# Kernel optimization log

Hardware: AMD Instinct MI355X
Metric: run time of the kernel (lower is better)

## Reference

```python
import jax, jax.numpy as jnp
import numpy as np

B, T, D, R = 8, 4096, 768, 16
DB = D // 3  # bucket size (d_img = d_sym = 256, d_rf = D - 2*DB = 256)


def setup_inputs() -> dict:
    key = jax.random.key(0)
    ks = jax.random.split(key, 10)
    s = 0.05
    x = jax.random.normal(ks[0], (B, T, D), dtype=jnp.float32)
    # torch nn.Linear stores weight as (out, in); y = x @ W.T + b
    V_w = jax.random.normal(ks[1], (R, D), dtype=jnp.float32) * s
    U_w = jax.random.normal(ks[2], (D, R), dtype=jnp.float32) * s
    E1_w = jax.random.normal(ks[3], (DB, D), dtype=jnp.float32) * s
    E1_b = jnp.zeros((DB,), dtype=jnp.float32)
    E2_w = jax.random.normal(ks[4], (3, DB), dtype=jnp.float32) * s
    E2_b = jnp.zeros((3,), dtype=jnp.float32)
    # a_base init per bucket: img=-0.6, sym=-1.0, rf=-1.6; a_delta init 0 (perturbed so tanh path is exercised)
    a_base = jnp.concatenate([
        jnp.full((DB,), -0.6, dtype=jnp.float32),
        jnp.full((DB,), -1.0, dtype=jnp.float32),
        jnp.full((D - 2 * DB,), -1.6, dtype=jnp.float32),
    ])
    a_delta = jax.random.normal(ks[5], (D,), dtype=jnp.float32) * 0.1
    C_w = jax.random.normal(ks[6], (D, D), dtype=jnp.float32) * s
    G_w = jax.random.normal(ks[7], (D, D), dtype=jnp.float32) * s
    G_b = jnp.zeros((D,), dtype=jnp.float32)
    return {"x": x, "V_w": V_w, "U_w": U_w, "E1_w": E1_w, "E1_b": E1_b,
            "E2_w": E2_w, "E2_b": E2_b, "a_base": a_base, "a_delta": a_delta,
            "C_w": C_w, "G_w": G_w, "G_b": G_b}


def reference(x, V_w, U_w, E1_w, E1_b, E2_w, E2_b, a_base, a_delta, C_w, G_w, G_b):
    d = x.shape[-1]
    db = d // 3
    # Low-rank input projection: Bu = U(V(x))
    Z = jnp.einsum('btd,rd->btr', x, V_w)            # (B,T,R)
    Bu = jnp.einsum('btr,dr->btd', Z, U_w)           # (B,T,D)
    # Evidence scores per timestep (3 clinical buckets)
    h = jax.nn.gelu(jnp.einsum('btd,ed->bte', x, E1_w) + E1_b, approximate=False)
    alpha = jax.nn.sigmoid(jnp.einsum('bte,ce->btc', h, E2_w) + E2_b)  # (B,T,3)
    # Broadcast each bucket's evidence score over its channels
    alpha_rep = jnp.concatenate([
        jnp.broadcast_to(alpha[..., 0:1], alpha.shape[:-1] + (db,)),
        jnp.broadcast_to(alpha[..., 1:2], alpha.shape[:-1] + (db,)),
        jnp.broadcast_to(alpha[..., 2:3], alpha.shape[:-1] + (d - 2 * db,)),
    ], axis=-1)                                       # (B,T,D)
    a_eff = a_base + alpha_rep * jnp.tanh(a_delta)    # (B,T,D)
    lam = jnp.exp(-jax.nn.softplus(-a_eff))           # (B,T,D), in (0,1)
    # Diagonal linear recurrence s_t = lam_t * s_{t-1} + Bu_t  (scan over time)
    def step(s, inp):
        l_t, bu_t = inp
        s = l_t * s + bu_t
        return s, s
    s0 = jnp.zeros(x.shape[:1] + x.shape[2:], dtype=x.dtype)  # (B,D)
    _, S = jax.lax.scan(step, s0, (jnp.swapaxes(lam, 0, 1), jnp.swapaxes(Bu, 0, 1)))
    S = jnp.swapaxes(S, 0, 1)                         # (B,T,D)
    y = jnp.einsum('btd,od->bto', S, C_w)
    gate = jax.nn.sigmoid(jnp.einsum('btd,od->bto', x, G_w) + G_b)
    y = jax.nn.gelu(y, approximate=False) * gate
    return x + y  # dropout is identity in eval mode
```

## Files before the change

kernel.cpp:

```cpp
#include <hip/hip_runtime.h>
#include <hip/hip_bf16.h>
#include <math.h>

#define B_   8
#define T_   4096
#define D_   768
#define R_   16
#define DB_  256
#define N_   (B_ * T_)
#define NC_  64
#define L_   (T_ / NC_)
#define NKS_ (D_ / 32)
#define BUF_  12288
#define BUFE_ 8192

typedef __attribute__((ext_vector_type(8))) short bf16x8;
typedef __attribute__((ext_vector_type(4))) float f32x4;

__device__ __forceinline__ float gelu_exact(float x) {
    return 0.5f * x * (1.0f + erff(x * 0.70710678118654752f));
}
__device__ __forceinline__ float sigmoidf_(float x) {
    return 1.0f / (1.0f + expf(-x));
}
__device__ __forceinline__ float bf2f(unsigned short u) {
    return __uint_as_float(((unsigned)u) << 16);
}
__device__ __forceinline__ unsigned short f2bf(float f) {
    __hip_bfloat16 h = __float2bfloat16(f);
    return *(unsigned short*)&h;
}
__device__ __forceinline__ bf16x8 pack8(float4 a, float4 b) {
    bf16x8 r;
    r[0] = (short)f2bf(a.x); r[1] = (short)f2bf(a.y);
    r[2] = (short)f2bf(a.z); r[3] = (short)f2bf(a.w);
    r[4] = (short)f2bf(b.x); r[5] = (short)f2bf(b.y);
    r[6] = (short)f2bf(b.z); r[7] = (short)f2bf(b.w);
    return r;
}

__device__ __forceinline__ void gload16(const unsigned short* g, unsigned short* l) {
    __builtin_amdgcn_global_load_lds(
        (const __attribute__((address_space(1))) unsigned int*)(const void*)g,
        (__attribute__((address_space(3))) unsigned int*)(void*)l,
        16, 0, 0);
}

__device__ __forceinline__ bf16x8 frag_read(const unsigned short* lds, int row, int lq) {
    int q = lq ^ ((row >> 1) & 3);
    return *(const bf16x8*)(lds + row * 32 + q * 8);
}

__device__ __forceinline__ void tile_decode(int nwg, int ncol, int& rowt, int& colt) {
    int bid = blockIdx.x;
    int cpx = nwg >> 3;
    int swz = (bid & 7) * cpx + (bid >> 3);
    colt = swz % ncol;
    rowt = swz / ncol;
}

__device__ __forceinline__ void stage_a(const unsigned short* src, int row0, int k0,
                                        unsigned short* lds, int w, int l) {
#pragma unroll
    for (int j = 0; j < 2; ++j) {
        int i = ((w * 2 + j) << 6) + l;
        int row = i >> 2, q = i & 3;
        int qs = q ^ ((row >> 1) & 3);
        gload16(src + (size_t)(row0 + row) * D_ + k0 + qs * 8, lds + ((w * 2 + j) << 9));
    }
}
__device__ __forceinline__ void stage_b(const unsigned short* src, int col0, int k0,
                                        unsigned short* lds, int w, int l) {
    int i = (w << 6) + l;
    int row = i >> 2, q = i & 3;
    int qs = q ^ ((row >> 1) & 3);
    gload16(src + (size_t)(col0 + row) * D_ + k0 + qs * 8, lds + (w << 9));
}

__device__ __forceinline__ void tile_mfma44(const unsigned short* la, const unsigned short* lb,
                                            int wrow, int wcol, int lr, int lq,
                                            f32x4 acc[4][4]) {
    bf16x8 a[4], b[4];
#pragma unroll
    for (int m = 0; m < 4; m++) a[m] = frag_read(la, wrow + m * 16 + lr, lq);
#pragma unroll
    for (int n = 0; n < 4; n++) b[n] = frag_read(lb, wcol + n * 16 + lr, lq);
    __builtin_amdgcn_s_setprio(1);
#pragma unroll
    for (int m = 0; m < 4; m++)
#pragma unroll
        for (int n = 0; n < 4; n++)
            acc[m][n] = __builtin_amdgcn_mfma_f32_16x16x32_bf16(a[m], b[n], acc[m][n], 0, 0, 0);
    __builtin_amdgcn_s_setprio(0);
}

__device__ __forceinline__ void prologueF(const unsigned short* __restrict__ A,
                                          const unsigned short* __restrict__ Bm,
                                          int row0, int col0,
                                          unsigned short* lds, int w, int l) {
    stage_a(A,  row0, 0,  lds,                w, l);
    stage_b(Bm, col0, 0,  lds + 8192,         w, l);
    stage_a(A,  row0, 32, lds + BUF_,         w, l);
    stage_b(Bm, col0, 32, lds + BUF_ + 8192,  w, l);
}

template <bool DO_PROLOGUE>
__device__ __forceinline__ void kloopF(const unsigned short* __restrict__ A,
                                       const unsigned short* __restrict__ Bm,
                                       int row0, int col0,
                                       unsigned short* lds,
                                       int w, int l, f32x4 acc[4][4]) {
    const int lr = l & 15, lq = l >> 4;
    const int wrow = (w >> 1) * 64, wcol = (w & 1) * 64;

    if (DO_PROLOGUE) prologueF(A, Bm, row0, col0, lds, w, l);

#pragma unroll 3
    for (int t = 0; t < NKS_ - 2; ++t) {
        asm volatile("s_waitcnt vmcnt(3)" ::: "memory");
        __builtin_amdgcn_s_barrier();
        __builtin_amdgcn_sched_barrier(0);
        unsigned short* bn = lds + ((t + 2) % 3) * BUF_;
        stage_a(A,  row0, (t + 2) * 32, bn,        w, l);
        stage_b(Bm, col0, (t + 2) * 32, bn + 8192, w, l);
        unsigned short* bc = lds + (t % 3) * BUF_;
        tile_mfma44(bc, bc + 8192, wrow, wcol, lr, lq, acc);
    }
    asm volatile("s_waitcnt vmcnt(3)" ::: "memory");
    __builtin_amdgcn_s_barrier();
    __builtin_amdgcn_sched_barrier(0);
    {
        unsigned short* bc = lds + ((NKS_ - 2) % 3) * BUF_;
        tile_mfma44(bc, bc + 8192, wrow, wcol, lr, lq, acc);
    }
    asm volatile("s_waitcnt vmcnt(0)" ::: "memory");
    __builtin_amdgcn_s_barrier();
    __builtin_amdgcn_sched_barrier(0);
    {
        unsigned short* bc = lds + ((NKS_ - 1) % 3) * BUF_;
        tile_mfma44(bc, bc + 8192, wrow, wcol, lr, lq, acc);
    }
}

__global__ __launch_bounds__(512, 2)
void gemm_fused_out(const unsigned short* __restrict__ Xb,
                    const unsigned short* __restrict__ Gwb,
                    const unsigned short* __restrict__ Sb,
                    const unsigned short* __restrict__ Cwb,
                    const float* __restrict__ Gbias,
                    float* __restrict__ out) {
    __shared__ unsigned short lds[3 * BUF_];
    const int t = threadIdx.x, l = t & 63, w = t >> 6;
    int rowt, colt;
    tile_decode(768, 6, rowt, colt);
    const int row0 = rowt * 256, col0 = colt * 128;
    const int lr = l & 15, lq = l >> 4;
    const int wrow = (w >> 1) * 64, wcol = (w & 1) * 64;

    float gb[4];
#pragma unroll
    for (int n = 0; n < 4; n++) gb[n] = Gbias[col0 + wcol + n * 16 + lr];

    f32x4 acc[4][4] = {};
    kloopF<true>(Xb, Gwb, row0, col0, lds, w, l, acc);

    prologueF(Sb, Cwb, row0, col0, lds, w, l);

    unsigned int gp[4][4][2];
#pragma unroll
    for (int m = 0; m < 4; m++)
#pragma unroll
        for (int n = 0; n < 4; n++) {
            gp[m][n][0] = (unsigned)f2bf(sigmoidf_(acc[m][n][0] + gb[n]))
                        | ((unsigned)f2bf(sigmoidf_(acc[m][n][1] + gb[n])) << 16);
            gp[m][n][1] = (unsigned)f2bf(sigmoidf_(acc[m][n][2] + gb[n]))
                        | ((unsigned)f2bf(sigmoidf_(acc[m][n][3] + gb[n])) << 16);
            acc[m][n] = (f32x4){0.f, 0.f, 0.f, 0.f};
        }

    kloopF<false>(Sb, Cwb, row0, col0, lds, w, l, acc);

#pragma unroll
    for (int m = 0; m < 4; m++)
#pragma unroll
        for (int n = 0; n < 4; n++) {
            int col = col0 + wcol + n * 16 + lr;
#pragma unroll
            for (int r = 0; r < 4; r++) {
                int row = row0 + wrow + m * 16 + lq * 4 + r;
                size_t o = (size_t)row * D_ + col;
                float g = bf2f((unsigned short)(gp[m][n][r >> 1] >> ((r & 1) * 16)));
                out[o] = bf2f(Xb[o]) + gelu_exact(acc[m][n][r]) * g;
            }
        }
}

__device__ __forceinline__ void stage_e(const unsigned short* __restrict__ A,
                                        const unsigned short* __restrict__ Bm,
                                        int row0, int col0, int k0,
                                        unsigned short* buf, int w, int l) {
    int i = (w << 6) + l;
    int row = i >> 2, q = i & 3;
    int qs = q ^ ((row >> 1) & 3);
    gload16(A  + (size_t)(row0 + row) * D_ + k0 + qs * 8, buf + (w << 9));
    gload16(Bm + (size_t)(col0 + row) * D_ + k0 + qs * 8, buf + 4096 + (w << 9));
}

__device__ __forceinline__ void tile_mfma24(const unsigned short* buf,
                                            int wrow, int wcol, int lr, int lq,
                                            f32x4 acc[2][4]) {
    const unsigned short* la = buf;
    const unsigned short* lb = buf + 4096;
    bf16x8 a[2], b[4];
#pragma unroll
    for (int m = 0; m < 2; m++) a[m] = frag_read(la, wrow + m * 16 + lr, lq);
#pragma unroll
    for (int n = 0; n < 4; n++) b[n] = frag_read(lb, wcol + n * 16 + lr, lq);
    __builtin_amdgcn_s_setprio(1);
#pragma unroll
    for (int m = 0; m < 2; m++)
#pragma unroll
        for (int n = 0; n < 4; n++)
            acc[m][n] = __builtin_amdgcn_mfma_f32_16x16x32_bf16(a[m], b[n], acc[m][n], 0, 0, 0);
    __builtin_amdgcn_s_setprio(0);
}

__device__ __forceinline__ void kloopE(const unsigned short* __restrict__ A,
                                       const unsigned short* __restrict__ Bm,
                                       int row0, int col0,
                                       unsigned short* lds,
                                       int w, int l, f32x4 acc[2][4]) {
    const int lr = l & 15, lq = l >> 4;
    const int wrow = (w >> 1) * 32, wcol = (w & 1) * 64;

    stage_e(A, Bm, row0, col0, 0,  lds,             w, l);
    stage_e(A, Bm, row0, col0, 32, lds + BUFE_,     w, l);
    stage_e(A, Bm, row0, col0, 64, lds + 2 * BUFE_, w, l);

#pragma unroll 4
    for (int t = 0; t < NKS_ - 3; ++t) {
        asm volatile("s_waitcnt vmcnt(4)" ::: "memory");
        __builtin_amdgcn_s_barrier();
        __builtin_amdgcn_sched_barrier(0);
        stage_e(A, Bm, row0, col0, (t + 3) * 32, lds + ((t + 3) & 3) * BUFE_, w, l);
        tile_mfma24(lds + (t & 3) * BUFE_, wrow, wcol, lr, lq, acc);
    }
    asm volatile("s_waitcnt vmcnt(4)" ::: "memory");
    __builtin_amdgcn_s_barrier();
    __builtin_amdgcn_sched_barrier(0);
    tile_mfma24(lds + ((NKS_ - 3) & 3) * BUFE_, wrow, wcol, lr, lq, acc);
    asm volatile("s_waitcnt vmcnt(2)" ::: "memory");
    __builtin_amdgcn_s_barrier();
    __builtin_amdgcn_sched_barrier(0);
    tile_mfma24(lds + ((NKS_ - 2) & 3) * BUFE_, wrow, wcol, lr, lq, acc);
    asm volatile("s_waitcnt vmcnt(0)" ::: "memory");
    __builtin_amdgcn_s_barrier();
    __builtin_amdgcn_sched_barrier(0);
    tile_mfma24(lds + ((NKS_ - 1) & 3) * BUFE_, wrow, wcol, lr, lq, acc);
}

__global__ __launch_bounds__(512, 2)
void gemm_e1_alpha(const unsigned short* __restrict__ Xb,
                   const unsigned short* __restrict__ Wb,
                   const float* __restrict__ bias,
                   const float* __restrict__ E2w,
                   float* __restrict__ alpha_acc) {
    __shared__ unsigned short lds[4 * BUFE_];
    const int t = threadIdx.x, l = t & 63, w = t >> 6;
    int rowt, colt;
    tile_decode(512, 2, rowt, colt);
    const int row0 = rowt * 128, col0 = colt * 128;
    const int lr = l & 15, lq = l >> 4;
    const int wrow = (w >> 1) * 32, wcol = (w & 1) * 64;
    f32x4 acc[2][4] = {};
    kloopE(Xb, Wb, row0, col0, lds, w, l, acc);

    float bia[4], e2v[3][4];
#pragma unroll
    for (int n = 0; n < 4; n++) {
        int col = col0 + wcol + n * 16 + lr;
        bia[n] = bias[col];
#pragma unroll
        for (int c = 0; c < 3; c++) e2v[c][n] = E2w[c * DB_ + col];
    }
#pragma unroll
    for (int m = 0; m < 2; m++)
#pragma unroll
        for (int r = 0; r < 4; r++) {
            float p0 = 0.f, p1 = 0.f, p2 = 0.f;
#pragma unroll
            for (int n = 0; n < 4; n++) {
                float h = gelu_exact(acc[m][n][r] + bia[n]);
                p0 = fmaf(h, e2v[0][n], p0);
                p1 = fmaf(h, e2v[1][n], p1);
                p2 = fmaf(h, e2v[2][n], p2);
            }
#pragma unroll
            for (int s = 1; s < 16; s <<= 1) {
                p0 += __shfl_xor(p0, s);
                p1 += __shfl_xor(p1, s);
                p2 += __shfl_xor(p2, s);
            }
            if (lr == 0) {
                int row = row0 + wrow + m * 16 + lq * 4 + r;
                atomicAdd(&alpha_acc[(size_t)row * 3 + 0], p0);
                atomicAdd(&alpha_acc[(size_t)row * 3 + 1], p1);
                atomicAdd(&alpha_acc[(size_t)row * 3 + 2], p2);
            }
        }
}

#define SEG_E1  (DB_ * D_ / 4)
#define SEG_W   (D_ * D_ / 4)
#define SEG_Z   (N_ * 3 / 4)
#define SEG_TOT (SEG_E1 + 2 * SEG_W + SEG_Z + 192)

__global__ __launch_bounds__(256)
void cvtz_kernel(const float* __restrict__ X, const float* __restrict__ Vw,
                 unsigned short* __restrict__ Xb, float* __restrict__ Z,
                 const float* __restrict__ E1_w, const float* __restrict__ C_w,
                 const float* __restrict__ G_w, const float* __restrict__ a_delta,
                 unsigned short* __restrict__ E1b, unsigned short* __restrict__ Cwb,
                 unsigned short* __restrict__ Gwb, float* __restrict__ al_acc,
                 float* __restrict__ tanhd) {
    const int t = threadIdx.x, l = t & 63, w = t >> 6;
    const int lr = l & 15, lq = l >> 4;
    const int tok0 = (blockIdx.x * 4 + w) * 16;
    const float* xrow = X  + (size_t)(tok0 + lr) * D_;
    const float* vrow = Vw + (size_t)lr * D_;
    f32x4 acc = {};
#pragma unroll 4
    for (int k0 = 0; k0 < D_; k0 += 32) {
        int k = k0 + lq * 8;
        float4 xa = *(const float4*)&xrow[k];
        float4 xb = *(const float4*)&xrow[k + 4];
        float4 va = *(const float4*)&vrow[k];
        float4 vb = *(const float4*)&vrow[k + 4];
        bf16x8 xf = pack8(xa, xb);
        bf16x8 vf = pack8(va, vb);
        *(bf16x8*)&Xb[(size_t)(tok0 + lr) * D_ + k] = xf;
        acc = __builtin_amdgcn_mfma_f32_16x16x32_bf16(xf, vf, acc, 0, 0, 0);
    }
#pragma unroll
    for (int rr = 0; rr < 4; rr++)
        Z[(size_t)(tok0 + lq * 4 + rr) * R_ + lr] = acc[rr];

    for (int i = blockIdx.x * 256 + t; i < SEG_TOT; i += 512 * 256) {
        if (i < SEG_E1) {
            float4 v = ((const float4*)E1_w)[i];
            ((ushort4*)E1b)[i] = make_ushort4(f2bf(v.x), f2bf(v.y), f2bf(v.z), f2bf(v.w));
        } else if (i < SEG_E1 + SEG_W) {
            int j = i - SEG_E1;
            float4 v = ((const float4*)C_w)[j];
            ((ushort4*)Cwb)[j] = make_ushort4(f2bf(v.x), f2bf(v.y), f2bf(v.z), f2bf(v.w));
        } else if (i < SEG_E1 + 2 * SEG_W) {
            int j = i - SEG_E1 - SEG_W;
            float4 v = ((const float4*)G_w)[j];
            ((ushort4*)Gwb)[j] = make_ushort4(f2bf(v.x), f2bf(v.y), f2bf(v.z), f2bf(v.w));
        } else if (i < SEG_E1 + 2 * SEG_W + SEG_Z) {
            int j = i - SEG_E1 - 2 * SEG_W;
            ((float4*)al_acc)[j] = make_float4(0.f, 0.f, 0.f, 0.f);
        } else {
            int j = (i - SEG_E1 - 2 * SEG_W - SEG_Z) * 4;
            tanhd[j + 0] = tanhf(a_delta[j + 0]);
            tanhd[j + 1] = tanhf(a_delta[j + 1]);
            tanhd[j + 2] = tanhf(a_delta[j + 2]);
            tanhd[j + 3] = tanhf(a_delta[j + 3]);
        }
    }
}

__device__ __forceinline__ void load_chunk_lds768(const float* __restrict__ Z,
                                                  const float* __restrict__ al_acc,
                                                  const float* __restrict__ E2b,
                                                  int tok0, int t,
                                                  float* Zs, float* als) {
    if (t < L_ * R_ / 4)
        ((float4*)Zs)[t] = ((const float4*)&Z[(size_t)tok0 * R_])[t];
    if (t < L_ * 3)
        als[t] = sigmoidf_(al_acc[(size_t)tok0 * 3 + t] + E2b[t % 3]);
}

__device__ __forceinline__ float dot16(const float* zrow, const float4* u) {
    float4 z0 = *(const float4*)&zrow[0],  z1 = *(const float4*)&zrow[4];
    float4 z2 = *(const float4*)&zrow[8],  z3 = *(const float4*)&zrow[12];
    return z0.x*u[0].x + z0.y*u[0].y + z0.z*u[0].z + z0.w*u[0].w
         + z1.x*u[1].x + z1.y*u[1].y + z1.z*u[1].z + z1.w*u[1].w
         + z2.x*u[2].x + z2.y*u[2].y + z2.z*u[2].z + z2.w*u[2].w
         + z3.x*u[3].x + z3.y*u[3].y + z3.z*u[3].z + z3.w*u[3].w;
}

__global__ __launch_bounds__(768, 2)
void scan_pass1(const float* __restrict__ Z, const float* __restrict__ al_acc,
                const float* __restrict__ E2b,
                const float* __restrict__ Uw, const float* __restrict__ a_base,
                const float* __restrict__ tanhd,
                float* __restrict__ Aagg, float* __restrict__ Send) {
    __shared__ float Zs[L_ * R_];
    __shared__ float als[L_ * 3];
    const int t = threadIdx.x;
    const int c = blockIdx.x & (NC_ - 1);
    const int b = blockIdx.x >> 6;
    const int tok0 = b * T_ + c * L_;
    const int buck = t >> 8;
    load_chunk_lds768(Z, al_acc, E2b, tok0, t, Zs, als);

    float4 u[4];
#pragma unroll
    for (int q = 0; q < 4; q++)
        u[q] = *(const float4*)&Uw[(size_t)t * R_ + q * 4];
    float ab = a_base[t];
    float td = tanhd[t];
    __syncthreads();

    float a = 1.f, s = 0.f;
    for (int i = 0; i < L_; i++) {
        float av  = als[i * 3 + buck];
        float lam = sigmoidf_(fmaf(av, td, ab));
        float bu  = dot16(&Zs[i * R_], u);
        a *= lam;
        s = fmaf(lam, s, bu);
    }
    size_t o = ((size_t)(b * NC_ + c)) * D_ + t;
    Aagg[o] = a;
    Send[o] = s;
}

__global__ __launch_bounds__(768, 2)
void scan_pass3(const float* __restrict__ Z, const float* __restrict__ al_acc,
                const float* __restrict__ E2b,
                const float* __restrict__ Uw, const float* __restrict__ a_base,
                const float* __restrict__ tanhd,
                const float* __restrict__ Aagg, const float* __restrict__ Send,
                unsigned short* __restrict__ Sout) {
    __shared__ float Zs[L_ * R_];
    __shared__ float als[L_ * 3];
    const int t = threadIdx.x;
    const int c = blockIdx.x & (NC_ - 1);
    const int b = blockIdx.x >> 6;
    const int tok0 = b * T_ + c * L_;
    const int buck = t >> 8;
    load_chunk_lds768(Z, al_acc, E2b, tok0, t, Zs, als);

    float4 u[4];
#pragma unroll
    for (int q = 0; q < 4; q++)
        u[q] = *(const float4*)&Uw[(size_t)t * R_ + q * 4];
    float ab = a_base[t];
    float td = tanhd[t];

    float s = 0.f;
#pragma unroll 4
    for (int cc = 0; cc < c; ++cc) {
        size_t o = ((size_t)(b * NC_ + cc)) * D_ + t;
        s = fmaf(Aagg[o], s, Send[o]);
    }
    __syncthreads();

    for (int i = 0; i < L_; i++) {
        float av  = als[i * 3 + buck];
        float lam = sigmoidf_(fmaf(av, td, ab));
        float bu  = dot16(&Zs[i * R_], u);
        s = fmaf(lam, s, bu);
        Sout[(size_t)(tok0 + i) * D_ + t] = f2bf(s);
    }
}

extern "C" void kernel_launch(void* const* d_in, const int* in_sizes, int n_in,
                              void* d_out, int out_size, void* d_ws, size_t ws_size,
                              hipStream_t stream) {
    const float* x       = (const float*)d_in[0];
    const float* V_w     = (const float*)d_in[1];
    const float* U_w     = (const float*)d_in[2];
    const float* E1_w    = (const float*)d_in[3];
    const float* E1_b    = (const float*)d_in[4];
    const float* E2_w    = (const float*)d_in[5];
    const float* E2_b    = (const float*)d_in[6];
    const float* a_base  = (const float*)d_in[7];
    const float* a_delta = (const float*)d_in[8];
    const float* C_w     = (const float*)d_in[9];
    const float* G_w     = (const float*)d_in[10];
    const float* G_b     = (const float*)d_in[11];
    float* out = (float*)d_out;

    char* p = (char*)d_ws;
    float* Aagg   = (float*)p;          p += (size_t)B_ * NC_ * D_ * 4;
    float* Send   = (float*)p;          p += (size_t)B_ * NC_ * D_ * 4;
    float* tanhd  = (float*)p;          p += (size_t)D_ * 4;
    float* Z      = (float*)p;          p += (size_t)N_ * R_ * 4;
    float* al_acc = (float*)p;          p += (size_t)N_ * 3 * 4;
    unsigned short* x_bf  = (unsigned short*)p; p += (size_t)N_ * D_ * 2;
    unsigned short* S_bf  = (unsigned short*)p; p += (size_t)N_ * D_ * 2;
    unsigned short* E1_bf = (unsigned short*)p; p += (size_t)DB_ * D_ * 2;
    unsigned short* Cw_bf = (unsigned short*)p; p += (size_t)D_ * D_ * 2;
    unsigned short* Gw_bf = (unsigned short*)p; p += (size_t)D_ * D_ * 2;

    cvtz_kernel<<<N_ / 64, 256, 0, stream>>>(x, V_w, x_bf, Z,
                                             E1_w, C_w, G_w, a_delta,
                                             E1_bf, Cw_bf, Gw_bf, al_acc, tanhd);

    gemm_e1_alpha<<<512, 512, 0, stream>>>(x_bf, E1_bf, E1_b, E2_w, al_acc);

    scan_pass1<<<B_ * NC_, 768, 0, stream>>>(Z, al_acc, E2_b, U_w, a_base, tanhd, Aagg, Send);
    scan_pass3<<<B_ * NC_, 768, 0, stream>>>(Z, al_acc, E2_b, U_w, a_base, tanhd, Aagg, Send, S_bf);

    gemm_fused_out<<<768, 512, 0, stream>>>(x_bf, Gw_bf, S_bf, Cw_bf, G_b, out);
}
```

Baseline: 276.6 us.

## Fuse two-pass chunked scan into one kernel with inter-block flag synchronization

Merges the chunk-aggregate pass and the carry-propagate pass of the time scan into a single kernel. Each block publishes its chunk aggregate, sets a flag, then spins until all earlier chunks of the same batch are flagged before computing its carry and writing the outputs. Flags are zeroed in the conversion kernel. This removes one kernel launch and the re-load of Z/alpha into LDS, but it relies on all 512 blocks being co-resident (768 threads, 2 per CU) to avoid deadlock, and it adds spin-wait latency.

```diff
diff --git a/kernel.cpp b/kernel.cpp
--- a/kernel.cpp
+++ b/kernel.cpp
@@ -313,7 +313,8 @@
 #define SEG_E1  (DB_ * D_ / 4)
 #define SEG_W   (D_ * D_ / 4)
 #define SEG_Z   (N_ * 3 / 4)
-#define SEG_TOT (SEG_E1 + 2 * SEG_W + SEG_Z + 192)
+#define SEG_F   (B_ * NC_ / 4)
+#define SEG_TOT (SEG_E1 + 2 * SEG_W + SEG_Z + SEG_F + 192)
 
 __global__ __launch_bounds__(256)
 void cvtz_kernel(const float* __restrict__ X, const float* __restrict__ Vw,
@@ -322,7 +323,7 @@
                  const float* __restrict__ G_w, const float* __restrict__ a_delta,
                  unsigned short* __restrict__ E1b, unsigned short* __restrict__ Cwb,
                  unsigned short* __restrict__ Gwb, float* __restrict__ al_acc,
-                 float* __restrict__ tanhd) {
+                 int* __restrict__ flags, float* __restrict__ tanhd) {
     const int t = threadIdx.x, l = t & 63, w = t >> 6;
     const int lr = l & 15, lq = l >> 4;
     const int tok0 = (blockIdx.x * 4 + w) * 16;
@@ -360,8 +361,11 @@
         } else if (i < SEG_E1 + 2 * SEG_W + SEG_Z) {
             int j = i - SEG_E1 - 2 * SEG_W;
             ((float4*)al_acc)[j] = make_float4(0.f, 0.f, 0.f, 0.f);
+        } else if (i < SEG_E1 + 2 * SEG_W + SEG_Z + SEG_F) {
+            int j = i - SEG_E1 - 2 * SEG_W - SEG_Z;
+            ((int4*)flags)[j] = make_int4(0, 0, 0, 0);
         } else {
-            int j = (i - SEG_E1 - 2 * SEG_W - SEG_Z) * 4;
+            int j = (i - SEG_E1 - 2 * SEG_W - SEG_Z - SEG_F) * 4;
             tanhd[j + 0] = tanhf(a_delta[j + 0]);
             tanhd[j + 1] = tanhf(a_delta[j + 1]);
             tanhd[j + 2] = tanhf(a_delta[j + 2]);
@@ -391,47 +395,12 @@
 }
 
 __global__ __launch_bounds__(768, 2)
-void scan_pass1(const float* __restrict__ Z, const float* __restrict__ al_acc,
+void scan_fused(const float* __restrict__ Z, const float* __restrict__ al_acc,
                 const float* __restrict__ E2b,
                 const float* __restrict__ Uw, const float* __restrict__ a_base,
                 const float* __restrict__ tanhd,
-                float* __restrict__ Aagg, float* __restrict__ Send) {
-    __shared__ float Zs[L_ * R_];
-    __shared__ float als[L_ * 3];
-    const int t = threadIdx.x;
-    const int c = blockIdx.x & (NC_ - 1);
-    const int b = blockIdx.x >> 6;
-    const int tok0 = b * T_ + c * L_;
-    const int buck = t >> 8;
-    load_chunk_lds768(Z, al_acc, E2b, tok0, t, Zs, als);
-
-    float4 u[4];
-#pragma unroll
-    for (int q = 0; q < 4; q++)
-        u[q] = *(const float4*)&Uw[(size_t)t * R_ + q * 4];
-    float ab = a_base[t];
-    float td = tanhd[t];
-    __syncthreads();
-
-    float a = 1.f, s = 0.f;
-    for (int i = 0; i < L_; i++) {
-        float av  = als[i * 3 + buck];
-        float lam = sigmoidf_(fmaf(av, td, ab));
-        float bu  = dot16(&Zs[i * R_], u);
-        a *= lam;
-        s = fmaf(lam, s, bu);
-    }
-    size_t o = ((size_t)(b * NC_ + c)) * D_ + t;
-    Aagg[o] = a;
-    Send[o] = s;
-}
-
-__global__ __launch_bounds__(768, 2)
-void scan_pass3(const float* __restrict__ Z, const float* __restrict__ al_acc,
-                const float* __restrict__ E2b,
-                const float* __restrict__ Uw, const float* __restrict__ a_base,
-                const float* __restrict__ tanhd,
-                const float* __restrict__ Aagg, const float* __restrict__ Send,
+                float* __restrict__ Aagg, float* __restrict__ Send,
+                int* __restrict__ flags,
                 unsigned short* __restrict__ Sout) {
     __shared__ float Zs[L_ * R_];
     __shared__ float als[L_ * 3];
@@ -448,21 +417,46 @@
         u[q] = *(const float4*)&Uw[(size_t)t * R_ + q * 4];
     float ab = a_base[t];
     float td = tanhd[t];
-
-    float s = 0.f;
-#pragma unroll 4
-    for (int cc = 0; cc < c; ++cc) {
-        size_t o = ((size_t)(b * NC_ + cc)) * D_ + t;
-        s = fmaf(Aagg[o], s, Send[o]);
-    }
     __syncthreads();
 
+    float a = 1.f, s = 0.f;
     for (int i = 0; i < L_; i++) {
         float av  = als[i * 3 + buck];
         float lam = sigmoidf_(fmaf(av, td, ab));
         float bu  = dot16(&Zs[i * R_], u);
+        a *= lam;
         s = fmaf(lam, s, bu);
-        Sout[(size_t)(tok0 + i) * D_ + t] = f2bf(s);
+    }
+    size_t o = ((size_t)(b * NC_ + c)) * D_ + t;
+    Aagg[o] = a;
+    Send[o] = s;
+    __syncthreads();
+    if (t == 0) {
+        __threadfence();
+        atomicExch(&flags[b * NC_ + c], 1);
+    }
+
+    float carry = 0.f;
+    if (c > 0) {
+        if (t == 0) {
+            for (int cc = 0; cc < c; ++cc)
+                while (atomicAdd(&flags[b * NC_ + cc], 0) == 0) { }
+        }
+        __syncthreads();
+        __threadfence();
+        for (int cc = 0; cc < c; ++cc) {
+            size_t oc = ((size_t)(b * NC_ + cc)) * D_ + t;
+            carry = fmaf(Aagg[oc], carry, Send[oc]);
+        }
+    }
+
+    float sf = carry;
+    for (int i = 0; i < L_; i++) {
+        float av  = als[i * 3 + buck];
+        float lam = sigmoidf_(fmaf(av, td, ab));
+        float bu  = dot16(&Zs[i * R_], u);
+        sf = fmaf(lam, sf, bu);
+        Sout[(size_t)(tok0 + i) * D_ + t] = f2bf(sf);
     }
 }
 
@@ -489,6 +483,7 @@
     float* tanhd  = (float*)p;          p += (size_t)D_ * 4;
     float* Z      = (float*)p;          p += (size_t)N_ * R_ * 4;
     float* al_acc = (float*)p;          p += (size_t)N_ * 3 * 4;
+    int*   flags  = (int*)p;            p += (size_t)B_ * NC_ * 4;
     unsigned short* x_bf  = (unsigned short*)p; p += (size_t)N_ * D_ * 2;
     unsigned short* S_bf  = (unsigned short*)p; p += (size_t)N_ * D_ * 2;
     unsigned short* E1_bf = (unsigned short*)p; p += (size_t)DB_ * D_ * 2;
@@ -497,12 +492,12 @@
 
     cvtz_kernel<<<N_ / 64, 256, 0, stream>>>(x, V_w, x_bf, Z,
                                              E1_w, C_w, G_w, a_delta,
-                                             E1_bf, Cw_bf, Gw_bf, al_acc, tanhd);
+                                             E1_bf, Cw_bf, Gw_bf, al_acc, flags, tanhd);
 
     gemm_e1_alpha<<<512, 512, 0, stream>>>(x_bf, E1_bf, E1_b, E2_w, al_acc);
 
-    scan_pass1<<<B_ * NC_, 768, 0, stream>>>(Z, al_acc, E2_b, U_w, a_base, tanhd, Aagg, Send);
-    scan_pass3<<<B_ * NC_, 768, 0, stream>>>(Z, al_acc, E2_b, U_w, a_base, tanhd, Aagg, Send, S_bf);
+    scan_fused<<<B_ * NC_, 768, 0, stream>>>(Z, al_acc, E2_b, U_w, a_base, tanhd,
+                                             Aagg, Send, flags, S_bf);
 
     gemm_fused_out<<<768, 512, 0, stream>>>(x_bf, Gw_bf, S_bf, Cw_bf, G_b, out);
 }
```

After: 426.7 us. 54.3% more time.
